# Kernel tuning notes

Measured on AMD Instinct MI355X. Metric: run time of the kernel, lower is better.

Reference implementation:

```python
import jax, jax.numpy as jnp
import numpy as np

B, N, D_IN, D_OUT, H = 8, 1024, 768, 768, 12
D_HEAD = D_OUT // H  # 64; per-head softmax scale is sqrt(D_HEAD)


def setup_inputs() -> dict:
    key = jax.random.key(0)
    kx, kq, kk, kv, kwo, kbo = jax.random.split(key, 6)
    s_in = 1.0 / np.sqrt(D_IN)
    s_out = 1.0 / np.sqrt(D_OUT)
    return {
        "x": jax.random.normal(kx, (B, N, D_IN), dtype=jnp.float32),
        # stacked per-head Linear weights, torch layout [out, in] -> [H, d_head, D_IN]
        "Wq": jax.random.uniform(kq, (H, D_HEAD, D_IN), jnp.float32, -s_in, s_in),
        "Wk": jax.random.uniform(kk, (H, D_HEAD, D_IN), jnp.float32, -s_in, s_in),
        "Wv": jax.random.uniform(kv, (H, D_HEAD, D_IN), jnp.float32, -s_in, s_in),
        "Wo": jax.random.uniform(kwo, (D_OUT, D_OUT), jnp.float32, -s_out, s_out),
        "bo": jax.random.uniform(kbo, (D_OUT,), jnp.float32, -s_out, s_out),
    }


def reference(x, Wq, Wk, Wv, Wo, bo):
    # Per-head projections, batched over heads: [B, H, N, d_head]
    q = jnp.einsum('bnd,hed->bhne', x, Wq)
    k = jnp.einsum('bnd,hed->bhne', x, Wk)
    v = jnp.einsum('bnd,hed->bhne', x, Wv)
    scale = 1.0 / np.sqrt(D_HEAD)
    scores = jnp.einsum('bhie,bhje->bhij', q, k) * scale  # [B, H, N, N]
    att = jax.nn.softmax(scores, axis=-1)
    out = jnp.einsum('bhij,bhje->bhie', att, v)  # [B, H, N, d_head]
    # concat heads along last dim: [B, N, H*d_head]
    out = out.transpose(0, 2, 1, 3).reshape(B, N, D_OUT)
    return out @ Wo.T + bo
```

## Files before the change

kernel.cpp:

```cpp
#include <hip/hip_runtime.h>
#include <hip/hip_bf16.h>


typedef unsigned short u16;
typedef __attribute__((ext_vector_type(8))) short bf8;
typedef __attribute__((ext_vector_type(4))) short bf4;
typedef __attribute__((ext_vector_type(4))) float f4;
typedef __attribute__((ext_vector_type(4))) unsigned short us4;

#define NB 8
#define NSEQ 1024
#define DMODEL 768
#define NHEAD 12
#define DHEAD 64

#define XELEMS   (NB * NSEQ * DMODEL)
#define WELEMS   (DMODEL * DMODEL)

#define PSTRIDE 132

__device__ __forceinline__ float b2f(u16 u) {
  union { unsigned int i; float f; } c; c.i = ((unsigned int)u) << 16; return c.f;
}
__device__ __forceinline__ u16 f2b(float f) {
  union { float f; unsigned int i; } c; c.f = f;
  unsigned int r = c.i + 0x7fffu + ((c.i >> 16) & 1u);
  return (u16)(r >> 16);
}
__device__ __forceinline__ void gl_lds16(const u16* g, u16* l) {
  __builtin_amdgcn_global_load_lds(
      (const __attribute__((address_space(1))) unsigned int*)g,
      (__attribute__((address_space(3))) unsigned int*)l, 16, 0, 0);
}

struct CvtArgs {
  const float* src[5];
  u16* dst[5];
};
#define G0 (XELEMS / 4)
#define GW (WELEMS / 4)
#define GTOT (G0 + 4 * GW)

__global__ __launch_bounds__(256) void cvt_kernel(CvtArgs a) {
  size_t g = (size_t)blockIdx.x * 256 + threadIdx.x;
  if (g >= GTOT) return;
  int t; size_t off;
  if (g < G0) { t = 0; off = g; }
  else { size_t r = g - G0; t = 1 + (int)(r / GW); off = r % GW; }
  f4 v = *(const f4*)(a.src[t] + off * 4);
  us4 o;
  o[0] = f2b(v[0]); o[1] = f2b(v[1]); o[2] = f2b(v[2]); o[3] = f2b(v[3]);
  *(us4*)(a.dst[t] + off * 4) = o;
}

__global__ __launch_bounds__(256) void qkv_gemm(
    const u16* __restrict__ x, const u16* __restrict__ Wq,
    const u16* __restrict__ Wk, const u16* __restrict__ Wv,
    u16* __restrict__ q, u16* __restrict__ k, u16* __restrict__ vt)
{
  __shared__ __align__(16) u16 lA[128 * 64];
  __shared__ __align__(16) u16 lB[128 * 64];

  const int tid  = threadIdx.x;
  const int lane = tid & 63;
  const int w    = tid >> 6;
  const int wm   = w >> 1, wn = w & 1;
  const int col  = lane & 15;
  const int quad = lane >> 4;
  const int bm = blockIdx.x;
  const int bn = blockIdx.y;

  const int m0 = bm * 128;
  const int proj = bn / 6;
  const u16* Wsel = (proj == 0) ? Wq : (proj == 1 ? Wk : Wv);
  const int nrem0 = (bn % 6) * 128;

  const int krow = lane >> 3;
  const int gsrc = (lane & 7) ^ krow;
  const u16* gA0 = x    + (size_t)(m0    + w * 32 + krow) * DMODEL + gsrc * 8;
  const u16* gB0 = Wsel + (size_t)(nrem0 + w * 32 + krow) * DMODEL + gsrc * 8;

  f4 acc[4][4];
#pragma unroll
  for (int i = 0; i < 4; i++)
#pragma unroll
    for (int j = 0; j < 4; j++) acc[i][j] = (f4)0.0f;

  for (int kk = 0; kk < DMODEL; kk += 64) {
    __syncthreads();
#pragma unroll
    for (int i = 0; i < 4; i++) {
      gl_lds16(gA0 + (size_t)(i * 8) * DMODEL + kk, lA + (w * 32 + i * 8) * 64);
      gl_lds16(gB0 + (size_t)(i * 8) * DMODEL + kk, lB + (w * 32 + i * 8) * 64);
    }
    __syncthreads();

#pragma unroll
    for (int kt = 0; kt < 2; kt++) {
      bf8 af[4], bfr[4];
#pragma unroll
      for (int mt = 0; mt < 4; mt++) {
        const int row = wm * 64 + mt * 16 + col;
        af[mt] = *(const bf8*)&lA[row * 64 + (((kt * 4 + quad) ^ (row & 7)) << 3)];
      }
#pragma unroll
      for (int nt = 0; nt < 4; nt++) {
        const int row = wn * 64 + nt * 16 + col;
        bfr[nt] = *(const bf8*)&lB[row * 64 + (((kt * 4 + quad) ^ (row & 7)) << 3)];
      }
#pragma unroll
      for (int mt = 0; mt < 4; mt++)
#pragma unroll
        for (int nt = 0; nt < 4; nt++)
          acc[mt][nt] = __builtin_amdgcn_mfma_f32_16x16x32_bf16(af[mt], bfr[nt], acc[mt][nt], 0, 0, 0);
    }
  }

  const int mw0 = m0 + wm * 64, nw0 = nrem0 + wn * 64;
  if (proj == 2) {
#pragma unroll
    for (int mt = 0; mt < 4; mt++) {
#pragma unroll
      for (int nt = 0; nt < 4; nt++) {
        const int nc = nw0 + nt * 16 + col;
        const int h = nc >> 6, e = nc & 63;
        const int t0 = mw0 + mt * 16 + quad * 4;
        const int b = t0 >> 10, tok0 = t0 & 1023;
        us4 pk;
#pragma unroll
        for (int r = 0; r < 4; r++) pk[r] = f2b(acc[mt][nt][r]);
        *(us4*)(vt + ((size_t)(b * NHEAD + h) * DHEAD + e) * NSEQ + tok0) = pk;
      }
    }
  } else {
    u16* dst = (proj == 0) ? q : k;
#pragma unroll
    for (int mt = 0; mt < 4; mt++) {
#pragma unroll
      for (int nt = 0; nt < 4; nt++) {
        const int nc = nw0 + nt * 16 + col;
        const int h = nc >> 6, e = nc & 63;
#pragma unroll
        for (int r = 0; r < 4; r++) {
          const int t = mw0 + mt * 16 + quad * 4 + r;
          const int b = t >> 10, tok = t & 1023;
          dst[((size_t)(b * NHEAD + h) * NSEQ + tok) * DHEAD + e] = f2b(acc[mt][nt][r]);
        }
      }
    }
  }
}

__global__ __launch_bounds__(256) void attn_kernel(
    const u16* __restrict__ q, const u16* __restrict__ k,
    const u16* __restrict__ vt, u16* __restrict__ attn)
{
  __shared__ __align__(16) u16 ldsK[128 * 64];
  __shared__ __align__(16) u16 ldsV[64 * 128];
  __shared__ __align__(16) u16 ldsP[4][16][PSTRIDE];

  const int tid  = threadIdx.x;
  const int lane = tid & 63;
  const int w    = tid >> 6;
  const int col  = lane & 15;
  const int quad = lane >> 4;

  const int idx = blockIdx.x;
  const int bh = idx % 96, qc = idx / 96;
  const int b = bh / 12, h = bh % 12;

  const size_t head = ((size_t)b * NHEAD + h) * NSEQ * DHEAD;
  const int q0 = qc * 128 + w * 32;

  const int krow = lane >> 3;
  const int kgsw = (lane & 7) ^ krow;
  const int vrow = lane >> 4;

  bf8 qf[2][2];
#pragma unroll
  for (int mt = 0; mt < 2; mt++)
#pragma unroll
    for (int kt = 0; kt < 2; kt++) {
      const int row = q0 + mt * 16 + col;
      bf8 t = *(const bf8*)(q + head + (size_t)row * DHEAD + kt * 32 + quad * 8);
#pragma unroll
      for (int j = 0; j < 8; j++) t[j] = (short)f2b(b2f((u16)t[j]) * 0.125f);
      qf[mt][kt] = t;
    }

  float l_[2][4];
  f4 o[2][4];
#pragma unroll
  for (int mt = 0; mt < 2; mt++) {
#pragma unroll
    for (int r = 0; r < 4; r++) l_[mt][r] = 0.0f;
#pragma unroll
    for (int et = 0; et < 4; et++) o[mt][et] = (f4)0.0f;
  }

  for (int t = 0; t < NSEQ / 128; t++) {
    const int kbase = t * 128;

    __syncthreads();
#pragma unroll
    for (int i = 0; i < 4; i++) {
      const int li = w * 4 + i;
      gl_lds16(k + head + (size_t)(kbase + li * 8 + krow) * DHEAD + kgsw * 8,
               &ldsK[li * 512]);
      const int vr = li * 4 + vrow;
      const int vgsw = (lane & 15) ^ (vr & 7);
      gl_lds16(vt + head + (size_t)vr * NSEQ + kbase + vgsw * 8,
               &ldsV[li * 512]);
    }
    __syncthreads();

    f4 s[2][8];
#pragma unroll
    for (int mt = 0; mt < 2; mt++)
#pragma unroll
      for (int nt = 0; nt < 8; nt++) s[mt][nt] = (f4)0.0f;
#pragma unroll
    for (int kt = 0; kt < 2; kt++) {
      bf8 kf[8];
#pragma unroll
      for (int nt = 0; nt < 8; nt++) {
        const int row = nt * 16 + col;
        kf[nt] = *(const bf8*)&ldsK[row * 64 + (((kt * 4 + quad) ^ (col & 7)) << 3)];
      }
#pragma unroll
      for (int mt = 0; mt < 2; mt++)
#pragma unroll
        for (int nt = 0; nt < 8; nt++)
          s[mt][nt] = __builtin_amdgcn_mfma_f32_16x16x32_bf16(qf[mt][kt], kf[nt], s[mt][nt], 0, 0, 0);
    }

#pragma unroll
    for (int mt = 0; mt < 2; mt++) {
#pragma unroll
      for (int nt = 0; nt < 8; nt++)
#pragma unroll
        for (int r = 0; r < 4; r++) {
          const float p = __expf(s[mt][nt][r]);
          l_[mt][r] += p;
          ldsP[w][quad * 4 + r][nt * 16 + col] = f2b(p);
        }
#pragma unroll
      for (int kt2 = 0; kt2 < 4; kt2++) {
        bf8 pf, vf[4];
        {
          const u16* pp = &ldsP[w][col][kt2 * 32 + quad * 8];
          bf4 lo = *(const bf4*)pp;
          bf4 hi = *(const bf4*)(pp + 4);
          pf = bf8{lo[0], lo[1], lo[2], lo[3], hi[0], hi[1], hi[2], hi[3]};
        }
#pragma unroll
        for (int et = 0; et < 4; et++) {
          const int row = et * 16 + col;
          vf[et] = *(const bf8*)&ldsV[row * 128 + (((kt2 * 4 + quad) ^ (col & 7)) << 3)];
        }
#pragma unroll
        for (int et = 0; et < 4; et++)
          o[mt][et] = __builtin_amdgcn_mfma_f32_16x16x32_bf16(pf, vf[et], o[mt][et], 0, 0, 0);
      }
    }
  }

#pragma unroll
  for (int mt = 0; mt < 2; mt++)
#pragma unroll
    for (int r = 0; r < 4; r++) {
      float sum = l_[mt][r];
      sum += __shfl_xor(sum, 1, 64);
      sum += __shfl_xor(sum, 2, 64);
      sum += __shfl_xor(sum, 4, 64);
      sum += __shfl_xor(sum, 8, 64);
      const float inv = 1.0f / sum;
      const int token = q0 + mt * 16 + quad * 4 + r;
#pragma unroll
      for (int et = 0; et < 4; et++)
        attn[(size_t)(b * NSEQ + token) * DMODEL + h * DHEAD + et * 16 + col] =
            f2b(o[mt][et][r] * inv);
    }
}

__global__ __launch_bounds__(256) void out_gemm(
    const u16* __restrict__ attn, const u16* __restrict__ Wo,
    const float* __restrict__ bo, float* __restrict__ out)
{
  __shared__ __align__(16) u16 lA[128 * 64];
  __shared__ __align__(16) u16 lB[128 * 64];

  const int tid  = threadIdx.x;
  const int lane = tid & 63;
  const int w    = tid >> 6;
  const int wm   = w >> 1, wn = w & 1;
  const int col  = lane & 15;
  const int quad = lane >> 4;
  const int bm = blockIdx.x;
  const int bn = blockIdx.y;

  const int m0 = bm * 128;
  const int n0 = bn * 128;

  const int krow = lane >> 3;
  const int gsrc = (lane & 7) ^ krow;
  const u16* gA0 = attn + (size_t)(m0 + w * 32 + krow) * DMODEL + gsrc * 8;
  const u16* gB0 = Wo   + (size_t)(n0 + w * 32 + krow) * DMODEL + gsrc * 8;

  f4 acc[4][4];
#pragma unroll
  for (int i = 0; i < 4; i++)
#pragma unroll
    for (int j = 0; j < 4; j++) acc[i][j] = (f4)0.0f;

  for (int kk = 0; kk < DMODEL; kk += 64) {
    __syncthreads();
#pragma unroll
    for (int i = 0; i < 4; i++) {
      gl_lds16(gA0 + (size_t)(i * 8) * DMODEL + kk, lA + (w * 32 + i * 8) * 64);
      gl_lds16(gB0 + (size_t)(i * 8) * DMODEL + kk, lB + (w * 32 + i * 8) * 64);
    }
    __syncthreads();

#pragma unroll
    for (int kt = 0; kt < 2; kt++) {
      bf8 af[4], bfr[4];
#pragma unroll
      for (int mt = 0; mt < 4; mt++) {
        const int row = wm * 64 + mt * 16 + col;
        af[mt] = *(const bf8*)&lA[row * 64 + (((kt * 4 + quad) ^ (row & 7)) << 3)];
      }
#pragma unroll
      for (int nt = 0; nt < 4; nt++) {
        const int row = wn * 64 + nt * 16 + col;
        bfr[nt] = *(const bf8*)&lB[row * 64 + (((kt * 4 + quad) ^ (row & 7)) << 3)];
      }
#pragma unroll
      for (int mt = 0; mt < 4; mt++)
#pragma unroll
        for (int nt = 0; nt < 4; nt++)
          acc[mt][nt] = __builtin_amdgcn_mfma_f32_16x16x32_bf16(af[mt], bfr[nt], acc[mt][nt], 0, 0, 0);
    }
  }

  const int mw0 = m0 + wm * 64, nw0 = n0 + wn * 64;
#pragma unroll
  for (int mt = 0; mt < 4; mt++)
#pragma unroll
    for (int nt = 0; nt < 4; nt++) {
      const int n = nw0 + nt * 16 + col;
      const float bias = bo[n];
#pragma unroll
      for (int r = 0; r < 4; r++) {
        const int row = mw0 + mt * 16 + quad * 4 + r;
        out[(size_t)row * DMODEL + n] = acc[mt][nt][r] + bias;
      }
    }
}

extern "C" void kernel_launch(void* const* d_in, const int* in_sizes, int n_in,
                              void* d_out, int out_size, void* d_ws, size_t ws_size,
                              hipStream_t stream) {
  const float* x  = (const float*)d_in[0];
  const float* Wq = (const float*)d_in[1];
  const float* Wk = (const float*)d_in[2];
  const float* Wv = (const float*)d_in[3];
  const float* Wo = (const float*)d_in[4];
  const float* bo = (const float*)d_in[5];
  float* out = (float*)d_out;

  u16* xb   = (u16*)d_ws;
  u16* wqb  = xb  + XELEMS;
  u16* wkb  = wqb + WELEMS;
  u16* wvb  = wkb + WELEMS;
  u16* wob  = wvb + WELEMS;
  u16* q    = wob + WELEMS;
  u16* k    = q   + XELEMS;
  u16* vt   = k   + XELEMS;
  u16* attn = vt  + XELEMS;

  CvtArgs ca;
  ca.src[0] = x;  ca.src[1] = Wq;  ca.src[2] = Wk;  ca.src[3] = Wv;  ca.src[4] = Wo;
  ca.dst[0] = xb; ca.dst[1] = wqb; ca.dst[2] = wkb; ca.dst[3] = wvb; ca.dst[4] = wob;

  cvt_kernel<<<dim3((GTOT + 255) / 256), 256, 0, stream>>>(ca);
  qkv_gemm<<<dim3(64, 18), 256, 0, stream>>>(xb, wqb, wkb, wvb, q, k, vt);
  attn_kernel<<<dim3(768), 256, 0, stream>>>(q, k, vt, attn);
  out_gemm<<<dim3(64, 6), 256, 0, stream>>>(attn, wob, bo, out);
}
```

Baseline: 208.7 us.

## Shrink attention KV tile to 64, compute row sums via MFMA, raise occupancy

Attention now streams K/V in 64-key tiles instead of 128, which shrinks the LDS footprint and the score register array so more blocks can be resident per CU. The softmax denominator is accumulated by an extra MFMA of the bf16 P tile against a ones vector, which drops the scalar adds and the cross-lane shuffle reduction. All three kernels also get a min-blocks hint of 4 in launch_bounds. The cost is twice as many loop iterations and barriers, and the row sum is now taken from bf16-rounded probabilities rather than the fp32 values.

Result: faster. 197.9 us (-5.2%).

```diff
diff --git a/kernel.cpp b/kernel.cpp
--- a/kernel.cpp
+++ b/kernel.cpp
@@ -16,8 +16,6 @@
 
 #define XELEMS   (NB * NSEQ * DMODEL)
 #define WELEMS   (DMODEL * DMODEL)
-
-#define PSTRIDE 132
 
 __device__ __forceinline__ float b2f(u16 u) {
   union { unsigned int i; float f; } c; c.i = ((unsigned int)u) << 16; return c.f;
@@ -53,7 +51,7 @@
   *(us4*)(a.dst[t] + off * 4) = o;
 }
 
-__global__ __launch_bounds__(256) void qkv_gemm(
+__global__ __launch_bounds__(256, 4) void qkv_gemm(
     const u16* __restrict__ x, const u16* __restrict__ Wq,
     const u16* __restrict__ Wk, const u16* __restrict__ Wv,
     u16* __restrict__ q, u16* __restrict__ k, u16* __restrict__ vt)
@@ -151,13 +149,13 @@
   }
 }
 
-__global__ __launch_bounds__(256) void attn_kernel(
+__global__ __launch_bounds__(256, 4) void attn_kernel(
     const u16* __restrict__ q, const u16* __restrict__ k,
     const u16* __restrict__ vt, u16* __restrict__ attn)
 {
-  __shared__ __align__(16) u16 ldsK[128 * 64];
-  __shared__ __align__(16) u16 ldsV[64 * 128];
-  __shared__ __align__(16) u16 ldsP[4][16][PSTRIDE];
+  __shared__ __align__(16) u16 ldsK[64 * 64];
+  __shared__ __align__(16) u16 ldsV[64 * 64];
+  __shared__ __align__(16) u16 ldsP[4][16][72];
 
   const int tid  = threadIdx.x;
   const int lane = tid & 63;
@@ -172,9 +170,12 @@
   const size_t head = ((size_t)b * NHEAD + h) * NSEQ * DHEAD;
   const int q0 = qc * 128 + w * 32;
 
-  const int krow = lane >> 3;
-  const int kgsw = (lane & 7) ^ krow;
-  const int vrow = lane >> 4;
+  const int srow8 = lane >> 3;
+  const int sg    = (lane & 7) ^ srow8;
+
+  bf8 onesf;
+#pragma unroll
+  for (int j = 0; j < 8; j++) onesf[j] = (short)0x3F80;
 
   bf8 qf[2][2];
 #pragma unroll
@@ -188,64 +189,58 @@
       qf[mt][kt] = t;
     }
 
-  float l_[2][4];
+  f4 lacc[2];
   f4 o[2][4];
 #pragma unroll
   for (int mt = 0; mt < 2; mt++) {
-#pragma unroll
-    for (int r = 0; r < 4; r++) l_[mt][r] = 0.0f;
+    lacc[mt] = (f4)0.0f;
 #pragma unroll
     for (int et = 0; et < 4; et++) o[mt][et] = (f4)0.0f;
   }
 
-  for (int t = 0; t < NSEQ / 128; t++) {
-    const int kbase = t * 128;
-
-    __syncthreads();
-#pragma unroll
-    for (int i = 0; i < 4; i++) {
-      const int li = w * 4 + i;
-      gl_lds16(k + head + (size_t)(kbase + li * 8 + krow) * DHEAD + kgsw * 8,
+  for (int t = 0; t < NSEQ / 64; t++) {
+    const int kbase = t * 64;
+
+    __syncthreads();
+#pragma unroll
+    for (int i = 0; i < 2; i++) {
+      const int li = w * 2 + i;
+      gl_lds16(k  + head + (size_t)(kbase + li * 8 + srow8) * DHEAD + sg * 8,
                &ldsK[li * 512]);
-      const int vr = li * 4 + vrow;
-      const int vgsw = (lane & 15) ^ (vr & 7);
-      gl_lds16(vt + head + (size_t)vr * NSEQ + kbase + vgsw * 8,
+      gl_lds16(vt + head + (size_t)(li * 8 + srow8) * NSEQ + kbase + sg * 8,
                &ldsV[li * 512]);
     }
     __syncthreads();
 
-    f4 s[2][8];
+    f4 s[2][4];
 #pragma unroll
     for (int mt = 0; mt < 2; mt++)
 #pragma unroll
-      for (int nt = 0; nt < 8; nt++) s[mt][nt] = (f4)0.0f;
+      for (int nt = 0; nt < 4; nt++) s[mt][nt] = (f4)0.0f;
 #pragma unroll
     for (int kt = 0; kt < 2; kt++) {
-      bf8 kf[8];
-#pragma unroll
-      for (int nt = 0; nt < 8; nt++) {
+      bf8 kf[4];
+#pragma unroll
+      for (int nt = 0; nt < 4; nt++) {
         const int row = nt * 16 + col;
         kf[nt] = *(const bf8*)&ldsK[row * 64 + (((kt * 4 + quad) ^ (col & 7)) << 3)];
       }
 #pragma unroll
       for (int mt = 0; mt < 2; mt++)
 #pragma unroll
-        for (int nt = 0; nt < 8; nt++)
+        for (int nt = 0; nt < 4; nt++)
           s[mt][nt] = __builtin_amdgcn_mfma_f32_16x16x32_bf16(qf[mt][kt], kf[nt], s[mt][nt], 0, 0, 0);
     }
 
 #pragma unroll
     for (int mt = 0; mt < 2; mt++) {
 #pragma unroll
-      for (int nt = 0; nt < 8; nt++)
-#pragma unroll
-        for (int r = 0; r < 4; r++) {
-          const float p = __expf(s[mt][nt][r]);
-          l_[mt][r] += p;
-          ldsP[w][quad * 4 + r][nt * 16 + col] = f2b(p);
-        }
-#pragma unroll
-      for (int kt2 = 0; kt2 < 4; kt2++) {
+      for (int nt = 0; nt < 4; nt++)
+#pragma unroll
+        for (int r = 0; r < 4; r++)
+          ldsP[w][quad * 4 + r][nt * 16 + col] = f2b(__expf(s[mt][nt][r]));
+#pragma unroll
+      for (int kt2 = 0; kt2 < 2; kt2++) {
         bf8 pf, vf[4];
         {
           const u16* pp = &ldsP[w][col][kt2 * 32 + quad * 8];
@@ -253,10 +248,11 @@
           bf4 hi = *(const bf4*)(pp + 4);
           pf = bf8{lo[0], lo[1], lo[2], lo[3], hi[0], hi[1], hi[2], hi[3]};
         }
+        lacc[mt] = __builtin_amdgcn_mfma_f32_16x16x32_bf16(pf, onesf, lacc[mt], 0, 0, 0);
 #pragma unroll
         for (int et = 0; et < 4; et++) {
           const int row = et * 16 + col;
-          vf[et] = *(const bf8*)&ldsV[row * 128 + (((kt2 * 4 + quad) ^ (col & 7)) << 3)];
+          vf[et] = *(const bf8*)&ldsV[row * 64 + (((kt2 * 4 + quad) ^ (col & 7)) << 3)];
         }
 #pragma unroll
         for (int et = 0; et < 4; et++)
@@ -269,12 +265,7 @@
   for (int mt = 0; mt < 2; mt++)
 #pragma unroll
     for (int r = 0; r < 4; r++) {
-      float sum = l_[mt][r];
-      sum += __shfl_xor(sum, 1, 64);
-      sum += __shfl_xor(sum, 2, 64);
-      sum += __shfl_xor(sum, 4, 64);
-      sum += __shfl_xor(sum, 8, 64);
-      const float inv = 1.0f / sum;
+      const float inv = 1.0f / lacc[mt][r];
       const int token = q0 + mt * 16 + quad * 4 + r;
 #pragma unroll
       for (int et = 0; et < 4; et++)
@@ -283,7 +274,7 @@
     }
 }
 
-__global__ __launch_bounds__(256) void out_gemm(
+__global__ __launch_bounds__(256, 4) void out_gemm(
     const u16* __restrict__ attn, const u16* __restrict__ Wo,
     const float* __restrict__ bo, float* __restrict__ out)
 {
```
